# Performance work log

Measured on AMD Instinct MI355X. Metric: run time of the kernel, lower is better.

The kernel has to match this reference:

```python
import jax, jax.numpy as jnp
import numpy as np


def setup_inputs() -> dict:
    key = jax.random.key(0)
    k1, k2, k3 = jax.random.split(key, 3)
    bz, L, d = 16, 2048, 768
    seq_prev = jax.random.normal(k1, (bz, L, d), dtype=jnp.float32)
    seq_after = jax.random.normal(k2, (bz, L, d), dtype=jnp.float32)
    # Linear(in_feat=768, out_feat=768) params; W stored as [in_feat, out_feat]
    W = jax.random.normal(k3, (d, d), dtype=jnp.float32) * (1.0 / np.sqrt(d))
    b = jnp.zeros((d,), dtype=jnp.float32)
    return {"seq_prev": seq_prev, "seq_after": seq_after, "W": W, "b": b}


def reference(seq_prev, seq_after, W, b):
    # 1-layer feed-forward + ReLU applied to both sequences
    p = jax.nn.relu(seq_prev @ W + b)   # [bz, L1, out_feat]
    a = jax.nn.relu(seq_after @ W + b)  # [bz, L2, out_feat]
    # broadcast-mul + sum over feat == batched dot-product similarity
    sim_score = jnp.einsum('bld,bmd->blm', p, a)  # [bz, L1, L2]
    return sim_score
```

## Files before the change

### kernel.cpp

```cpp
#include <hip/hip_runtime.h>
#include <hip/hip_bf16.h>
#include <hip/hip_fp8.h>


typedef __attribute__((ext_vector_type(8)))  short bf16x8v;
typedef __attribute__((ext_vector_type(8)))  short s16x8;
typedef __attribute__((ext_vector_type(4)))  float f32x4;
typedef __attribute__((ext_vector_type(16))) float f32x16;
typedef __attribute__((ext_vector_type(4)))  float float4v;
typedef __attribute__((ext_vector_type(8)))  int   int8v;
typedef __attribute__((ext_vector_type(4)))  int   int4v;

__device__ __forceinline__ unsigned short f2bf(float f) {
  unsigned int u = __float_as_uint(f);
  u += 0x7fffu + ((u >> 16) & 1u);
  return (unsigned short)(u >> 16);
}

__device__ __forceinline__ unsigned char f2e4m3(float f) {
  __hip_fp8_e4m3 q(f);
  return (unsigned char)q.__x;
}

__device__ __forceinline__ void async_copy16(void* lds, const void* g) {
  __builtin_amdgcn_global_load_lds(
      (const __attribute__((address_space(1))) void*)g,
      (__attribute__((address_space(3))) void*)lds, 16, 0, 0);
}

#define BAR()    asm volatile("s_barrier" ::: "memory")
#define WAITV3() asm volatile("s_waitcnt vmcnt(3)" ::: "memory")
#define WAITV0() asm volatile("s_waitcnt vmcnt(0)" ::: "memory")
#define WAITL()  do { asm volatile("s_waitcnt lgkmcnt(0)" ::: "memory"); \
                      __builtin_amdgcn_sched_barrier(0); } while (0)
#define FBARF()   do { __builtin_amdgcn_sched_barrier(0);                 \
                       __builtin_amdgcn_s_barrier();                      \
                       __builtin_amdgcn_sched_barrier(0); } while (0)
#define FWAITV(n) do { asm volatile("s_waitcnt vmcnt(" #n ")" ::: "memory"); \
                       __builtin_amdgcn_sched_barrier(0); } while (0)
#define FLGKM0()  do { asm volatile("s_waitcnt lgkmcnt(0)" ::: "memory");  \
                       __builtin_amdgcn_sched_barrier(0); } while (0)

__global__ void wt_kernel(const float* __restrict__ W, short* __restrict__ Wt) {
  int idx = blockIdx.x * 256 + threadIdx.x;
  int n = idx / 768;
  int k = idx - n * 768;
  Wt[idx] = (short)f2bf(W[k * 768 + n]);
}

__global__ __launch_bounds__(512, 2)
void gemm_ff(const float* __restrict__ Sprev, const float* __restrict__ Safter,
             const short* __restrict__ Wt, const float* __restrict__ bias,
             unsigned char* __restrict__ Out) {
  constexpr int BK = 64, KT = 12;
  __shared__ __align__(16) short lA[2][256 * BK];
  __shared__ __align__(16) short lB[2][256 * BK];

  const int bid  = blockIdx.x;
  const int virt = (bid & 7) * 96 + (bid >> 3);
  const int by   = virt / 3;
  const int bx   = virt - by * 3;

  const int tid  = threadIdx.x;
  const int lane = tid & 63;
  const int w    = tid >> 6;
  const int wr   = w >> 2;
  const int wc   = w & 3;
  const int tn   = bx * 256;

  const float* Af = (by < 128 ? Sprev : Safter) + (size_t)((by & 127) * 256) * 768;
  const int    tm = by * 256;

  const int l31  = lane & 31;
  const int khb  = (lane >> 5) * 16;
  const int sx   = ((lane >> 2) & 7) << 4;
  const int arow = wr * 128 + l31;
  const int brow = wc * 64 + l31;

#define FF_LOAD_A(k0)                                                         \
  {                                                                           \
    _Pragma("unroll")                                                         \
    for (int _q = 0; _q < 4; ++_q) {                                          \
      int _seg = _q * 512 + tid;                                              \
      int _row = _seg >> 3;                                                   \
      const float* _g = Af + (size_t)_row * 768 + (k0) + (_seg & 7) * 8;      \
      ar[2 * _q]     = *(const float4v*)_g;                                   \
      ar[2 * _q + 1] = *(const float4v*)(_g + 4);                             \
    }                                                                         \
  }

#define FF_CVT_WRITE(buf)                                                     \
  {                                                                           \
    _Pragma("unroll")                                                         \
    for (int _q = 0; _q < 4; ++_q) {                                          \
      int _seg = _q * 512 + tid;                                              \
      int _row = _seg >> 3;                                                   \
      int _cb  = ((_seg & 7) * 16) ^ (((_row >> 2) & 7) << 4);                \
      s16x8 _o;                                                               \
      _o[0] = (short)f2bf(ar[2 * _q][0]);     _o[1] = (short)f2bf(ar[2 * _q][1]); \
      _o[2] = (short)f2bf(ar[2 * _q][2]);     _o[3] = (short)f2bf(ar[2 * _q][3]); \
      _o[4] = (short)f2bf(ar[2 * _q + 1][0]); _o[5] = (short)f2bf(ar[2 * _q + 1][1]); \
      _o[6] = (short)f2bf(ar[2 * _q + 1][2]); _o[7] = (short)f2bf(ar[2 * _q + 1][3]); \
      *(s16x8*)((char*)lA[buf] + _row * 128 + _cb) = _o;                      \
    }                                                                         \
  }

#define FF_STAGE_B(buf, k0)                                                   \
  {                                                                           \
    _Pragma("unroll")                                                         \
    for (int _j = 0; _j < 4; ++_j) {                                          \
      int _c   = _j * 512 + tid;                                              \
      int _row = _c >> 3;                                                     \
      int _cb  = ((_c & 7) * 16) ^ (((_row >> 2) & 7) << 4);                  \
      async_copy16((char*)lB[buf] + _j * 8192 + w * 1024,                     \
                   (const char*)(Wt + (size_t)(tn + _row) * 768 + (k0)) + _cb); \
    }                                                                         \
  }

#define FF_FRAGS(buf, kk)                                                     \
  {                                                                           \
    const char* _bA = (const char*)lA[buf];                                   \
    const char* _bB = (const char*)lB[buf];                                   \
    _Pragma("unroll")                                                         \
    for (int _ks = 0; _ks < 2; ++_ks) {                                       \
      const int _kx = ((kk) * 64 + _ks * 32 + khb) ^ sx;                      \
      _Pragma("unroll")                                                       \
      for (int _mt = 0; _mt < 4; ++_mt)                                       \
        af[_mt][_ks] = *(const bf16x8v*)(_bA + (arow + _mt * 32) * 128 + _kx);\
      _Pragma("unroll")                                                       \
      for (int _nt = 0; _nt < 2; ++_nt)                                       \
        bg[_nt][_ks] = *(const bf16x8v*)(_bB + (brow + _nt * 32) * 128 + _kx);\
    }                                                                         \
  }

#define FF_MFMA()                                                             \
  {                                                                           \
    __builtin_amdgcn_s_setprio(1);                                            \
    _Pragma("unroll")                                                         \
    for (int _ks = 0; _ks < 2; ++_ks)                                         \
      _Pragma("unroll")                                                       \
      for (int _mt = 0; _mt < 4; ++_mt)                                       \
        _Pragma("unroll")                                                     \
        for (int _nt = 0; _nt < 2; ++_nt)                                     \
          acc[_mt][_nt] = __builtin_amdgcn_mfma_f32_32x32x16_bf16(            \
              af[_mt][_ks], bg[_nt][_ks], acc[_mt][_nt], 0, 0, 0);            \
    __builtin_amdgcn_s_setprio(0);                                            \
  }

  f32x16 acc[4][2] = {};
  bf16x8v af[4][2], bg[2][2];
  float4v ar[8];

  FF_LOAD_A(0);
  FWAITV(0);
  FF_CVT_WRITE(0);
  FF_LOAD_A(BK);
  FF_STAGE_B(0, 0);
  FF_STAGE_B(1, BK);
  FLGKM0();
  FWAITV(4);
  FBARF();

  for (int kt = 0; kt < KT; ++kt) {
    const int cur = kt & 1, nxt = cur ^ 1;
    FF_FRAGS(cur, 0);
    if (kt + 1 < KT) {
      FWAITV(4);
      FF_CVT_WRITE(nxt);
    }
    FLGKM0();
    FF_MFMA();
    if (kt + 2 < KT) FF_LOAD_A((kt + 2) * BK);
    FF_FRAGS(cur, 1);
    FLGKM0();
    if (kt + 1 < KT) {
      if (kt + 2 < KT) { FWAITV(8); }
      else             { FWAITV(0); }
      FBARF();
      if (kt + 2 < KT) FF_STAGE_B(cur, (kt + 2) * BK);
    }
    FF_MFMA();
  }

#pragma unroll
  for (int mt = 0; mt < 4; ++mt) {
    int rowb = tm + wr * 128 + mt * 32 + 4 * (lane >> 5);
#pragma unroll
    for (int nt = 0; nt < 2; ++nt) {
      int col = tn + wc * 64 + nt * 32 + l31;
      float bv = bias[col];
#pragma unroll
      for (int reg = 0; reg < 16; ++reg) {
        int row = rowb + (reg & 3) + 8 * (reg >> 2);
        float v = fmaxf(acc[mt][nt][reg] + bv, 0.0f);
        Out[(size_t)row * 768 + col] = f2e4m3(v);
      }
    }
  }
#undef FF_LOAD_A
#undef FF_CVT_WRITE
#undef FF_STAGE_B
#undef FF_FRAGS
#undef FF_MFMA
}

__global__ __launch_bounds__(512, 4)
void gemm_sim(const unsigned char* __restrict__ A, const unsigned char* __restrict__ B,
              float* __restrict__ C) {
  constexpr int BK = 64, KT = 12, LD = 2048;
  __shared__ __align__(16) unsigned char lA[2][256 * BK];
  __shared__ __align__(16) unsigned char lB[2][128 * BK];

  const int bid  = blockIdx.x;
  const int virt = (bid & 7) * 256 + (bid >> 3);
  const int bz   = virt >> 7;
  const int rem  = virt & 127;
  const int by   = rem >> 4;
  const int bx   = rem & 15;

  const int tid  = threadIdx.x;
  const int lane = tid & 63;
  const int w    = tid >> 6;
  const int wr   = w >> 1;
  const int wc   = w & 1;
  const int tm   = by * 256;
  const int tn   = bx * 128;

  const unsigned char* Ab = A + (size_t)bz * LD * 768 + (size_t)tm * 768;
  const unsigned char* Bb = B + (size_t)bz * LD * 768 + (size_t)tn * 768;

  const int l31  = lane & 31;
  const int kq32 = (lane >> 5) * 32;
  const int arow = wr * 64 + l31;
  const int brow = wc * 64 + l31;
  const int swA  = ((arow >> 1) & 3) << 4;
  const int swB  = ((brow >> 1) & 3) << 4;

#define STAGE(buf, k0)                                                        \
  {                                                                           \
    _Pragma("unroll")                                                         \
    for (int _j = 0; _j < 2; ++_j) {                                          \
      int _c   = _j * 512 + tid;                                              \
      int _row = _c >> 2;                                                     \
      int _cb  = ((_c & 3) * 16) ^ (((_row >> 1) & 3) << 4);                  \
      async_copy16((char*)lA[buf] + _j * 8192 + w * 1024,                     \
                   Ab + (size_t)_row * 768 + (k0) + _cb);                     \
    }                                                                         \
    {                                                                         \
      int _row = tid >> 2;                                                    \
      int _cb  = ((tid & 3) * 16) ^ (((_row >> 1) & 3) << 4);                 \
      async_copy16((char*)lB[buf] + w * 1024,                                 \
                   Bb + (size_t)_row * 768 + (k0) + _cb);                     \
    }                                                                         \
  }

#define LOAD_FRAGS_ALL(buf)                                                   \
  {                                                                           \
    const char* _bA = (const char*)lA[buf];                                   \
    const char* _bB = (const char*)lB[buf];                                   \
    _Pragma("unroll")                                                         \
    for (int _mt = 0; _mt < 2; ++_mt) {                                       \
      const char* _r = _bA + (arow + _mt * 32) * BK;                          \
      int4v _lo = *(const int4v*)(_r + ((kq32 + 0)  ^ swA));                  \
      int4v _hi = *(const int4v*)(_r + ((kq32 + 16) ^ swA));                  \
      af[_mt][0] = _lo[0]; af[_mt][1] = _lo[1];                               \
      af[_mt][2] = _lo[2]; af[_mt][3] = _lo[3];                               \
      af[_mt][4] = _hi[0]; af[_mt][5] = _hi[1];                               \
      af[_mt][6] = _hi[2]; af[_mt][7] = _hi[3];                               \
    }                                                                         \
    _Pragma("unroll")                                                         \
    for (int _nt = 0; _nt < 2; ++_nt) {                                       \
      const char* _r = _bB + (brow + _nt * 32) * BK;                          \
      int4v _lo = *(const int4v*)(_r + ((kq32 + 0)  ^ swB));                  \
      int4v _hi = *(const int4v*)(_r + ((kq32 + 16) ^ swB));                  \
      bg[_nt][0] = _lo[0]; bg[_nt][1] = _lo[1];                               \
      bg[_nt][2] = _lo[2]; bg[_nt][3] = _lo[3];                               \
      bg[_nt][4] = _hi[0]; bg[_nt][5] = _hi[1];                               \
      bg[_nt][6] = _hi[2]; bg[_nt][7] = _hi[3];                               \
    }                                                                         \
  }

#define MFMA_ALL()                                                            \
  {                                                                           \
    __builtin_amdgcn_s_setprio(1);                                            \
    _Pragma("unroll")                                                         \
    for (int _mt = 0; _mt < 2; ++_mt)                                         \
      _Pragma("unroll")                                                       \
      for (int _nt = 0; _nt < 2; ++_nt)                                       \
        acc[_mt][_nt] = __builtin_amdgcn_mfma_scale_f32_32x32x64_f8f6f4(      \
            af[_mt], bg[_nt], acc[_mt][_nt], 0, 0, 0, 0x7F, 0, 0x7F);         \
    __builtin_amdgcn_s_setprio(0);                                            \
  }

  f32x16 acc[2][2] = {};
  int8v af[2], bg[2];

  STAGE(0, 0);
  STAGE(1, BK);

  int cur = 0;
  for (int kt = 0; kt < KT; ++kt) {
    if (kt < KT - 1) { WAITV3(); } else { WAITV0(); }
    BAR();

    LOAD_FRAGS_ALL(cur);
    WAITL();
    BAR();
    if (kt < KT - 2) STAGE(cur, (kt + 2) * BK);
    MFMA_ALL();

    cur ^= 1;
  }

  float* Cb = C + (size_t)bz * LD * LD;
#pragma unroll
  for (int mt = 0; mt < 2; ++mt) {
    int rowb = tm + wr * 64 + mt * 32 + 4 * (lane >> 5);
#pragma unroll
    for (int nt = 0; nt < 2; ++nt) {
      int col = tn + wc * 64 + nt * 32 + l31;
#pragma unroll
      for (int reg = 0; reg < 16; ++reg) {
        int row = rowb + (reg & 3) + 8 * (reg >> 2);
        Cb[(size_t)row * LD + col] = acc[mt][nt][reg];
      }
    }
  }
#undef STAGE
#undef LOAD_FRAGS_ALL
#undef MFMA_ALL
}

extern "C" void kernel_launch(void* const* d_in, const int* in_sizes, int n_in,
                              void* d_out, int out_size, void* d_ws, size_t ws_size,
                              hipStream_t stream) {
  const float* seq_prev  = (const float*)d_in[0];
  const float* seq_after = (const float*)d_in[1];
  const float* W         = (const float*)d_in[2];
  const float* bias      = (const float*)d_in[3];
  float* out             = (float*)d_out;

  char* ws           = (char*)d_ws;
  short* Wt          = (short*)ws;
  unsigned char* P8  = (unsigned char*)(ws + 1179648);

  constexpr int NSEQ = 16 * 2048 * 768;

  wt_kernel<<<768 * 768 / 256, 256, 0, stream>>>(W, Wt);

  gemm_ff<<<768, 512, 0, stream>>>(seq_prev, seq_after, Wt, bias, P8);

  gemm_sim<<<2048, 512, 0, stream>>>(P8, P8 + NSEQ, out);
}
```

Baseline: 217.4 us.

## Stage fp32 A tiles via async LDS copies and convert to bf16 at fragment read

The feed-forward GEMM now copies fp32 activations straight into LDS with async copies and converts them to bf16 right before each MFMA, instead of loading them into registers and converting before the LDS write. Tiles shrink from 256x256 with BK 64 to 256x128 with BK 32, and the grid doubles to 1536 blocks. Each wave computes a 64x64 subtile with fewer accumulators. The aim is to take register-staged global loads off the critical path and raise parallelism, at the cost of twice the LDS traffic for A, repeated conversion work, and more re-reads of A across N tiles.

```diff
diff --git a/kernel.cpp b/kernel.cpp
--- a/kernel.cpp
+++ b/kernel.cpp
@@ -52,139 +52,116 @@
 void gemm_ff(const float* __restrict__ Sprev, const float* __restrict__ Safter,
              const short* __restrict__ Wt, const float* __restrict__ bias,
              unsigned char* __restrict__ Out) {
-  constexpr int BK = 64, KT = 12;
-  __shared__ __align__(16) short lA[2][256 * BK];
-  __shared__ __align__(16) short lB[2][256 * BK];
+  constexpr int BK = 32, KT = 24;
+  __shared__ __align__(16) float lA[2][256 * BK];
+  __shared__ __align__(16) short lB[2][128 * BK];
 
   const int bid  = blockIdx.x;
-  const int virt = (bid & 7) * 96 + (bid >> 3);
-  const int by   = virt / 3;
-  const int bx   = virt - by * 3;
+  const int virt = (bid & 7) * 192 + (bid >> 3);
+  const int by   = virt / 6;
+  const int bx   = virt - by * 6;
 
   const int tid  = threadIdx.x;
   const int lane = tid & 63;
   const int w    = tid >> 6;
-  const int wr   = w >> 2;
-  const int wc   = w & 3;
-  const int tn   = bx * 256;
+  const int wr   = w >> 1;
+  const int wc   = w & 1;
+  const int tn   = bx * 128;
 
   const float* Af = (by < 128 ? Sprev : Safter) + (size_t)((by & 127) * 256) * 768;
   const int    tm = by * 256;
 
   const int l31  = lane & 31;
-  const int khb  = (lane >> 5) * 16;
-  const int sx   = ((lane >> 2) & 7) << 4;
-  const int arow = wr * 128 + l31;
+  const int khi  = lane >> 5;
+  const int arow = wr * 64 + l31;
   const int brow = wc * 64 + l31;
-
-#define FF_LOAD_A(k0)                                                         \
-  {                                                                           \
-    _Pragma("unroll")                                                         \
-    for (int _q = 0; _q < 4; ++_q) {                                          \
-      int _seg = _q * 512 + tid;                                              \
-      int _row = _seg >> 3;                                                   \
-      const float* _g = Af + (size_t)_row * 768 + (k0) + (_seg & 7) * 8;      \
-      ar[2 * _q]     = *(const float4v*)_g;                                   \
-      ar[2 * _q + 1] = *(const float4v*)(_g + 4);                             \
-    }                                                                         \
-  }
-
-#define FF_CVT_WRITE(buf)                                                     \
-  {                                                                           \
-    _Pragma("unroll")                                                         \
-    for (int _q = 0; _q < 4; ++_q) {                                          \
-      int _seg = _q * 512 + tid;                                              \
-      int _row = _seg >> 3;                                                   \
-      int _cb  = ((_seg & 7) * 16) ^ (((_row >> 2) & 7) << 4);                \
-      s16x8 _o;                                                               \
-      _o[0] = (short)f2bf(ar[2 * _q][0]);     _o[1] = (short)f2bf(ar[2 * _q][1]); \
-      _o[2] = (short)f2bf(ar[2 * _q][2]);     _o[3] = (short)f2bf(ar[2 * _q][3]); \
-      _o[4] = (short)f2bf(ar[2 * _q + 1][0]); _o[5] = (short)f2bf(ar[2 * _q + 1][1]); \
-      _o[6] = (short)f2bf(ar[2 * _q + 1][2]); _o[7] = (short)f2bf(ar[2 * _q + 1][3]); \
-      *(s16x8*)((char*)lA[buf] + _row * 128 + _cb) = _o;                      \
-    }                                                                         \
-  }
-
-#define FF_STAGE_B(buf, k0)                                                   \
+  const int swA  = (lane & 7) << 4;
+  const int swB  = ((brow >> 1) & 3) << 4;
+
+#define FF_STAGE(buf, k0)                                                     \
   {                                                                           \
     _Pragma("unroll")                                                         \
     for (int _j = 0; _j < 4; ++_j) {                                          \
       int _c   = _j * 512 + tid;                                              \
       int _row = _c >> 3;                                                     \
-      int _cb  = ((_c & 7) * 16) ^ (((_row >> 2) & 7) << 4);                  \
-      async_copy16((char*)lB[buf] + _j * 8192 + w * 1024,                     \
+      int _cb  = ((_c & 7) * 16) ^ ((_row & 7) << 4);                         \
+      async_copy16((char*)lA[buf] + _j * 8192 + w * 1024,                     \
+                   (const char*)(Af + (size_t)_row * 768 + (k0)) + _cb);      \
+    }                                                                         \
+    {                                                                         \
+      int _row = tid >> 2;                                                    \
+      int _cb  = ((tid & 3) * 16) ^ (((_row >> 1) & 3) << 4);                 \
+      async_copy16((char*)lB[buf] + w * 1024,                                 \
                    (const char*)(Wt + (size_t)(tn + _row) * 768 + (k0)) + _cb); \
     }                                                                         \
   }
 
-#define FF_FRAGS(buf, kk)                                                     \
+#define FF_READ(buf, ks)                                                      \
   {                                                                           \
     const char* _bA = (const char*)lA[buf];                                   \
     const char* _bB = (const char*)lB[buf];                                   \
     _Pragma("unroll")                                                         \
-    for (int _ks = 0; _ks < 2; ++_ks) {                                       \
-      const int _kx = ((kk) * 64 + _ks * 32 + khb) ^ sx;                      \
-      _Pragma("unroll")                                                       \
-      for (int _mt = 0; _mt < 4; ++_mt)                                       \
-        af[_mt][_ks] = *(const bf16x8v*)(_bA + (arow + _mt * 32) * 128 + _kx);\
+    for (int _mt = 0; _mt < 2; ++_mt) {                                       \
+      const char* _r = _bA + (arow + _mt * 32) * 128;                         \
+      raw[_mt][0] = *(const int4v*)(_r + (((ks) * 64 + khi * 32 + 0)  ^ swA));\
+      raw[_mt][1] = *(const int4v*)(_r + (((ks) * 64 + khi * 32 + 16) ^ swA));\
+    }                                                                         \
+    _Pragma("unroll")                                                         \
+    for (int _nt = 0; _nt < 2; ++_nt)                                         \
+      bg[_nt] = *(const bf16x8v*)(_bB + (brow + _nt * 32) * 64 +              \
+                                  (((ks) * 32 + khi * 16) ^ swB));            \
+  }
+
+#define FF_CVT_MFMA()                                                         \
+  {                                                                           \
+    bf16x8v _af[2];                                                           \
+    _Pragma("unroll")                                                         \
+    for (int _mt = 0; _mt < 2; ++_mt) {                                       \
+      float4v _f0 = *(float4v*)&raw[_mt][0];                                  \
+      float4v _f1 = *(float4v*)&raw[_mt][1];                                  \
+      s16x8 _o;                                                               \
+      _o[0] = (short)f2bf(_f0[0]); _o[1] = (short)f2bf(_f0[1]);               \
+      _o[2] = (short)f2bf(_f0[2]); _o[3] = (short)f2bf(_f0[3]);               \
+      _o[4] = (short)f2bf(_f1[0]); _o[5] = (short)f2bf(_f1[1]);               \
+      _o[6] = (short)f2bf(_f1[2]); _o[7] = (short)f2bf(_f1[3]);               \
+      _af[_mt] = (bf16x8v)_o;                                                 \
+    }                                                                         \
+    __builtin_amdgcn_s_setprio(1);                                            \
+    _Pragma("unroll")                                                         \
+    for (int _mt = 0; _mt < 2; ++_mt)                                         \
       _Pragma("unroll")                                                       \
       for (int _nt = 0; _nt < 2; ++_nt)                                       \
-        bg[_nt][_ks] = *(const bf16x8v*)(_bB + (brow + _nt * 32) * 128 + _kx);\
-    }                                                                         \
-  }
-
-#define FF_MFMA()                                                             \
-  {                                                                           \
-    __builtin_amdgcn_s_setprio(1);                                            \
-    _Pragma("unroll")                                                         \
-    for (int _ks = 0; _ks < 2; ++_ks)                                         \
-      _Pragma("unroll")                                                       \
-      for (int _mt = 0; _mt < 4; ++_mt)                                       \
-        _Pragma("unroll")                                                     \
-        for (int _nt = 0; _nt < 2; ++_nt)                                     \
-          acc[_mt][_nt] = __builtin_amdgcn_mfma_f32_32x32x16_bf16(            \
-              af[_mt][_ks], bg[_nt][_ks], acc[_mt][_nt], 0, 0, 0);            \
+        acc[_mt][_nt] = __builtin_amdgcn_mfma_f32_32x32x16_bf16(              \
+            _af[_mt], bg[_nt], acc[_mt][_nt], 0, 0, 0);                       \
     __builtin_amdgcn_s_setprio(0);                                            \
   }
 
-  f32x16 acc[4][2] = {};
-  bf16x8v af[4][2], bg[2][2];
-  float4v ar[8];
-
-  FF_LOAD_A(0);
-  FWAITV(0);
-  FF_CVT_WRITE(0);
-  FF_LOAD_A(BK);
-  FF_STAGE_B(0, 0);
-  FF_STAGE_B(1, BK);
-  FLGKM0();
-  FWAITV(4);
-  FBARF();
+  f32x16 acc[2][2] = {};
+  int4v  raw[2][2];
+  bf16x8v bg[2];
+
+  FF_STAGE(0, 0);
+  FF_STAGE(1, BK);
 
   for (int kt = 0; kt < KT; ++kt) {
-    const int cur = kt & 1, nxt = cur ^ 1;
-    FF_FRAGS(cur, 0);
-    if (kt + 1 < KT) {
-      FWAITV(4);
-      FF_CVT_WRITE(nxt);
-    }
+    const int cur = kt & 1;
+    if (kt < KT - 1) { FWAITV(5); } else { FWAITV(0); }
+    FBARF();
+
+    FF_READ(cur, 0);
     FLGKM0();
-    FF_MFMA();
-    if (kt + 2 < KT) FF_LOAD_A((kt + 2) * BK);
-    FF_FRAGS(cur, 1);
+    FF_CVT_MFMA();
+
+    FF_READ(cur, 1);
     FLGKM0();
-    if (kt + 1 < KT) {
-      if (kt + 2 < KT) { FWAITV(8); }
-      else             { FWAITV(0); }
-      FBARF();
-      if (kt + 2 < KT) FF_STAGE_B(cur, (kt + 2) * BK);
-    }
-    FF_MFMA();
-  }
-
-#pragma unroll
-  for (int mt = 0; mt < 4; ++mt) {
-    int rowb = tm + wr * 128 + mt * 32 + 4 * (lane >> 5);
+    FBARF();
+    if (kt + 2 < KT) FF_STAGE(cur, (kt + 2) * BK);
+    FF_CVT_MFMA();
+  }
+
+#pragma unroll
+  for (int mt = 0; mt < 2; ++mt) {
+    int rowb = tm + wr * 64 + mt * 32 + 4 * (lane >> 5);
 #pragma unroll
     for (int nt = 0; nt < 2; ++nt) {
       int col = tn + wc * 64 + nt * 32 + l31;
@@ -197,11 +174,9 @@
       }
     }
   }
-#undef FF_LOAD_A
-#undef FF_CVT_WRITE
-#undef FF_STAGE_B
-#undef FF_FRAGS
-#undef FF_MFMA
+#undef FF_STAGE
+#undef FF_READ
+#undef FF_CVT_MFMA
 }
 
 __global__ __launch_bounds__(512, 4)
@@ -348,7 +323,7 @@
 
   wt_kernel<<<768 * 768 / 256, 256, 0, stream>>>(W, Wt);
 
-  gemm_ff<<<768, 512, 0, stream>>>(seq_prev, seq_after, Wt, bias, P8);
+  gemm_ff<<<1536, 512, 0, stream>>>(seq_prev, seq_after, Wt, bias, P8);
 
   gemm_sim<<<2048, 512, 0, stream>>>(P8, P8 + NSEQ, out);
 }
```

Measured after the change: 247.4 us. 1.14x slower.

## Shrink feed-forward GEMM tiles to 128x256 with BK=32 for higher occupancy

Applied to the files above, without the earlier changes.

The feed-forward GEMM tile drops from 256x256 to 128x256 rows, BK is halved to 32 with twice as many k-steps, and the grid doubles to 1536 blocks. Launch bounds now target 4 blocks per CU and the accumulator and fragment register footprint shrinks. LDS swizzles and vmcnt waits are adjusted to the new 64-byte row pitch. The aim is more resident waves to hide global-load latency on the fp32 A operand, at the cost of lower arithmetic intensity, more barriers per unit of work, and re-reading W for each smaller tile.

```diff
diff --git a/kernel.cpp b/kernel.cpp
--- a/kernel.cpp
+++ b/kernel.cpp
@@ -48,16 +48,16 @@
   Wt[idx] = (short)f2bf(W[k * 768 + n]);
 }
 
-__global__ __launch_bounds__(512, 2)
+__global__ __launch_bounds__(512, 4)
 void gemm_ff(const float* __restrict__ Sprev, const float* __restrict__ Safter,
              const short* __restrict__ Wt, const float* __restrict__ bias,
              unsigned char* __restrict__ Out) {
-  constexpr int BK = 64, KT = 12;
-  __shared__ __align__(16) short lA[2][256 * BK];
+  constexpr int BK = 32, KT = 24;
+  __shared__ __align__(16) short lA[2][128 * BK];
   __shared__ __align__(16) short lB[2][256 * BK];
 
   const int bid  = blockIdx.x;
-  const int virt = (bid & 7) * 96 + (bid >> 3);
+  const int virt = (bid & 7) * 192 + (bid >> 3);
   const int by   = virt / 3;
   const int bx   = virt - by * 3;
 
@@ -68,88 +68,77 @@
   const int wc   = w & 3;
   const int tn   = bx * 256;
 
-  const float* Af = (by < 128 ? Sprev : Safter) + (size_t)((by & 127) * 256) * 768;
-  const int    tm = by * 256;
+  const float* Af = (by < 256 ? Sprev : Safter) + (size_t)((by & 255) * 128) * 768;
+  const int    tm = by * 128;
 
   const int l31  = lane & 31;
-  const int khb  = (lane >> 5) * 16;
-  const int sx   = ((lane >> 2) & 7) << 4;
-  const int arow = wr * 128 + l31;
+  const int khi  = lane >> 5;
+  const int arow = wr * 64 + l31;
   const int brow = wc * 64 + l31;
+  const int swA  = ((arow >> 1) & 3) << 4;
+  const int swB  = ((brow >> 1) & 3) << 4;
 
 #define FF_LOAD_A(k0)                                                         \
   {                                                                           \
-    _Pragma("unroll")                                                         \
-    for (int _q = 0; _q < 4; ++_q) {                                          \
-      int _seg = _q * 512 + tid;                                              \
-      int _row = _seg >> 3;                                                   \
-      const float* _g = Af + (size_t)_row * 768 + (k0) + (_seg & 7) * 8;      \
-      ar[2 * _q]     = *(const float4v*)_g;                                   \
-      ar[2 * _q + 1] = *(const float4v*)(_g + 4);                             \
-    }                                                                         \
+    int _row = tid >> 2;                                                      \
+    const float* _g = Af + (size_t)_row * 768 + (k0) + (tid & 3) * 8;         \
+    ar[0] = *(const float4v*)_g;                                              \
+    ar[1] = *(const float4v*)(_g + 4);                                        \
   }
 
 #define FF_CVT_WRITE(buf)                                                     \
   {                                                                           \
-    _Pragma("unroll")                                                         \
-    for (int _q = 0; _q < 4; ++_q) {                                          \
-      int _seg = _q * 512 + tid;                                              \
-      int _row = _seg >> 3;                                                   \
-      int _cb  = ((_seg & 7) * 16) ^ (((_row >> 2) & 7) << 4);                \
-      s16x8 _o;                                                               \
-      _o[0] = (short)f2bf(ar[2 * _q][0]);     _o[1] = (short)f2bf(ar[2 * _q][1]); \
-      _o[2] = (short)f2bf(ar[2 * _q][2]);     _o[3] = (short)f2bf(ar[2 * _q][3]); \
-      _o[4] = (short)f2bf(ar[2 * _q + 1][0]); _o[5] = (short)f2bf(ar[2 * _q + 1][1]); \
-      _o[6] = (short)f2bf(ar[2 * _q + 1][2]); _o[7] = (short)f2bf(ar[2 * _q + 1][3]); \
-      *(s16x8*)((char*)lA[buf] + _row * 128 + _cb) = _o;                      \
-    }                                                                         \
+    int _row = tid >> 2;                                                      \
+    int _cb  = ((tid & 3) * 16) ^ (((_row >> 1) & 3) << 4);                   \
+    s16x8 _o;                                                                 \
+    _o[0] = (short)f2bf(ar[0][0]); _o[1] = (short)f2bf(ar[0][1]);             \
+    _o[2] = (short)f2bf(ar[0][2]); _o[3] = (short)f2bf(ar[0][3]);             \
+    _o[4] = (short)f2bf(ar[1][0]); _o[5] = (short)f2bf(ar[1][1]);             \
+    _o[6] = (short)f2bf(ar[1][2]); _o[7] = (short)f2bf(ar[1][3]);             \
+    *(s16x8*)((char*)lA[buf] + _row * 64 + _cb) = _o;                         \
   }
 
 #define FF_STAGE_B(buf, k0)                                                   \
   {                                                                           \
     _Pragma("unroll")                                                         \
-    for (int _j = 0; _j < 4; ++_j) {                                          \
+    for (int _j = 0; _j < 2; ++_j) {                                          \
       int _c   = _j * 512 + tid;                                              \
-      int _row = _c >> 3;                                                     \
-      int _cb  = ((_c & 7) * 16) ^ (((_row >> 2) & 7) << 4);                  \
+      int _row = _c >> 2;                                                     \
+      int _cb  = ((_c & 3) * 16) ^ (((_row >> 1) & 3) << 4);                  \
       async_copy16((char*)lB[buf] + _j * 8192 + w * 1024,                     \
                    (const char*)(Wt + (size_t)(tn + _row) * 768 + (k0)) + _cb); \
     }                                                                         \
   }
 
-#define FF_FRAGS(buf, kk)                                                     \
+#define FF_FRAGS(buf, ks)                                                     \
   {                                                                           \
     const char* _bA = (const char*)lA[buf];                                   \
     const char* _bB = (const char*)lB[buf];                                   \
-    _Pragma("unroll")                                                         \
-    for (int _ks = 0; _ks < 2; ++_ks) {                                       \
-      const int _kx = ((kk) * 64 + _ks * 32 + khb) ^ sx;                      \
-      _Pragma("unroll")                                                       \
-      for (int _mt = 0; _mt < 4; ++_mt)                                       \
-        af[_mt][_ks] = *(const bf16x8v*)(_bA + (arow + _mt * 32) * 128 + _kx);\
+    const int _kxA = ((ks) * 32 + khi * 16) ^ swA;                            \
+    const int _kxB = ((ks) * 32 + khi * 16) ^ swB;                            \
+    _Pragma("unroll")                                                         \
+    for (int _mt = 0; _mt < 2; ++_mt)                                         \
+      af[_mt] = *(const bf16x8v*)(_bA + (arow + _mt * 32) * 64 + _kxA);       \
+    _Pragma("unroll")                                                         \
+    for (int _nt = 0; _nt < 2; ++_nt)                                         \
+      bg[_nt] = *(const bf16x8v*)(_bB + (brow + _nt * 32) * 64 + _kxB);       \
+  }
+
+#define FF_MFMA()                                                             \
+  {                                                                           \
+    __builtin_amdgcn_s_setprio(1);                                            \
+    _Pragma("unroll")                                                         \
+    for (int _mt = 0; _mt < 2; ++_mt)                                         \
       _Pragma("unroll")                                                       \
       for (int _nt = 0; _nt < 2; ++_nt)                                       \
-        bg[_nt][_ks] = *(const bf16x8v*)(_bB + (brow + _nt * 32) * 128 + _kx);\
-    }                                                                         \
-  }
-
-#define FF_MFMA()                                                             \
-  {                                                                           \
-    __builtin_amdgcn_s_setprio(1);                                            \
-    _Pragma("unroll")                                                         \
-    for (int _ks = 0; _ks < 2; ++_ks)                                         \
-      _Pragma("unroll")                                                       \
-      for (int _mt = 0; _mt < 4; ++_mt)                                       \
-        _Pragma("unroll")                                                     \
-        for (int _nt = 0; _nt < 2; ++_nt)                                     \
-          acc[_mt][_nt] = __builtin_amdgcn_mfma_f32_32x32x16_bf16(            \
-              af[_mt][_ks], bg[_nt][_ks], acc[_mt][_nt], 0, 0, 0);            \
+        acc[_mt][_nt] = __builtin_amdgcn_mfma_f32_32x32x16_bf16(              \
+            af[_mt], bg[_nt], acc[_mt][_nt], 0, 0, 0);                        \
     __builtin_amdgcn_s_setprio(0);                                            \
   }
 
-  f32x16 acc[4][2] = {};
-  bf16x8v af[4][2], bg[2][2];
-  float4v ar[8];
+  f32x16 acc[2][2] = {};
+  float4v ar[2];
+  bf16x8v af[2], bg[2];
 
   FF_LOAD_A(0);
   FWAITV(0);
@@ -158,14 +147,14 @@
   FF_STAGE_B(0, 0);
   FF_STAGE_B(1, BK);
   FLGKM0();
-  FWAITV(4);
+  FWAITV(2);
   FBARF();
 
   for (int kt = 0; kt < KT; ++kt) {
     const int cur = kt & 1, nxt = cur ^ 1;
     FF_FRAGS(cur, 0);
     if (kt + 1 < KT) {
-      FWAITV(4);
+      FWAITV(2);
       FF_CVT_WRITE(nxt);
     }
     FLGKM0();
@@ -174,7 +163,7 @@
     FF_FRAGS(cur, 1);
     FLGKM0();
     if (kt + 1 < KT) {
-      if (kt + 2 < KT) { FWAITV(8); }
+      if (kt + 2 < KT) { FWAITV(2); }
       else             { FWAITV(0); }
       FBARF();
       if (kt + 2 < KT) FF_STAGE_B(cur, (kt + 2) * BK);
@@ -183,8 +172,8 @@
   }
 
 #pragma unroll
-  for (int mt = 0; mt < 4; ++mt) {
-    int rowb = tm + wr * 128 + mt * 32 + 4 * (lane >> 5);
+  for (int mt = 0; mt < 2; ++mt) {
+    int rowb = tm + wr * 64 + mt * 32 + 4 * (lane >> 5);
 #pragma unroll
     for (int nt = 0; nt < 2; ++nt) {
       int col = tn + wc * 64 + nt * 32 + l31;
@@ -348,7 +337,7 @@
 
   wt_kernel<<<768 * 768 / 256, 256, 0, stream>>>(W, Wt);
 
-  gemm_ff<<<768, 512, 0, stream>>>(seq_prev, seq_after, Wt, bias, P8);
+  gemm_ff<<<1536, 512, 0, stream>>>(seq_prev, seq_after, Wt, bias, P8);
 
   gemm_sim<<<2048, 512, 0, stream>>>(P8, P8 + NSEQ, out);
 }
```

After: 215.8 us. About the same (-0.8%).
